# Optimization experiments

Measured on AMD Instinct MI355X. Metric: run time of the kernel, lower is better.

The kernel has to match this reference:

```python
import jax, jax.numpy as jnp
import numpy as np
from functools import partial

N_NODES = 100000
N_EDGES = 3200000
F_IN, H1, H2, C_OUT = 128, 64, 32, 2


def setup_inputs() -> dict:
    key = jax.random.key(0)
    ks = jax.random.split(key, 8)
    x = jax.random.normal(ks[0], (N_NODES, F_IN), dtype=jnp.float32)
    edge_index = jax.random.randint(ks[1], (2, N_EDGES), 0, N_NODES, dtype=jnp.int64)
    def glorot(k, fan_in, fan_out):
        s = jnp.sqrt(6.0 / (fan_in + fan_out))
        return jax.random.uniform(k, (fan_in, fan_out), jnp.float32, -s, s)
    return {
        "x": x,
        "edge_index": edge_index,
        "W1": glorot(ks[2], F_IN, H1), "b1": jnp.zeros((H1,), jnp.float32),
        "W2": glorot(ks[3], H1, H2),   "b2": jnp.zeros((H2,), jnp.float32),
        "W3": glorot(ks[4], H2, C_OUT), "b3": jnp.zeros((C_OUT,), jnp.float32),
    }


def _gcn_norm(edge_index, num_nodes):
    # add self-loops, compute symmetric normalization D^{-1/2} (A+I) D^{-1/2}
    loop = jnp.arange(num_nodes, dtype=edge_index.dtype)
    src = jnp.concatenate([edge_index[0], loop])
    dst = jnp.concatenate([edge_index[1], loop])
    deg = jax.ops.segment_sum(jnp.ones_like(dst, dtype=jnp.float32), dst,
                              num_segments=num_nodes)
    dinv = jax.lax.rsqrt(deg)  # deg >= 1 because of self-loops
    norm = dinv[src] * dinv[dst]  # [E + N]
    return src, dst, norm


def _gcn_conv(x, W, b, src, dst, norm, num_nodes):
    # PyG GCNConv: linear transform, then normalized scatter-aggregate, then bias
    xw = x @ W                                   # [N, F_out]
    msg = xw[src] * norm[:, None]                # [E+N, F_out] gather + scale
    out = jax.ops.segment_sum(msg, dst, num_segments=num_nodes)
    return out + b


def reference(x, edge_index, W1, b1, W2, b2, W3, b3):
    n = x.shape[0]
    src, dst, norm = _gcn_norm(edge_index, n)
    h = jax.nn.relu(_gcn_conv(x, W1, b1, src, dst, norm, n))
    # dropout is identity in eval mode
    h = jax.nn.relu(_gcn_conv(h, W2, b2, src, dst, norm, n))
    h = _gcn_conv(h, W3, b3, src, dst, norm, n)
    return jax.nn.log_softmax(h, axis=1)
```

## Files before the change

### kernel.cpp

```cpp
#include <hip/hip_runtime.h>
#include <hip/hip_bf16.h>
#include <math.h>

constexpr int N = 100000;
constexpr int E = 3200000;
constexpr int FIN = 128, H1 = 64, H2 = 32, COUT = 2;

constexpr int BUK_SHIFT = 8;
constexpr int BUK_NODES = 256;
constexpr int NBUK = (N + BUK_NODES - 1) / BUK_NODES;
constexpr int CAP = 10240;
constexpr int MS_TPB = 1024;
constexpr int MS_EPT = 12;
constexpr int CHUNK = MS_TPB * MS_EPT;
constexpr int MS_WGS = (E + CHUNK - 1) / CHUNK;

__global__ void k_initcur(int* __restrict__ gcursor) {
    int i = blockIdx.x * blockDim.x + threadIdx.x;
    if (i < NBUK) gcursor[i] = i * CAP;
}

__global__ __launch_bounds__(MS_TPB)
void k_mslice(const int* __restrict__ src, const int* __restrict__ dst,
              int* __restrict__ gcursor, unsigned* __restrict__ ebuf) {
    __shared__ int cnt[NBUK];
    __shared__ int base[NBUK];
    const int t = threadIdx.x;
    for (int i = t; i < NBUK; i += MS_TPB) cnt[i] = 0;
    __syncthreads();
    const int e0 = blockIdx.x * CHUNK;

    int rb[MS_EPT];
    unsigned rv[MS_EPT];
#pragma unroll
    for (int j = 0; j < MS_EPT; ++j) {
        int e = e0 + j * MS_TPB + t;
        if (e < E) {
            int d = dst[e];
            int b = d >> BUK_SHIFT;
            rb[j] = b;
            rv[j] = (unsigned)src[e] | ((unsigned)(d & (BUK_NODES - 1)) << 17);
            atomicAdd(&cnt[b], 1);
        } else {
            rb[j] = -1; rv[j] = 0;
        }
    }
    __syncthreads();
    for (int i = t; i < NBUK; i += MS_TPB) {
        int c = cnt[i];
        base[i] = c ? atomicAdd(&gcursor[i], c) : 0;
    }
    __syncthreads();
    for (int i = t; i < NBUK; i += MS_TPB) cnt[i] = 0;
    __syncthreads();
#pragma unroll
    for (int j = 0; j < MS_EPT; ++j) {
        int b = rb[j];
        if (b >= 0) {
            int r = atomicAdd(&cnt[b], 1);
            int p = base[b] + r;
            if (p < (b + 1) * CAP) ebuf[p] = rv[j];
        }
    }
}

__global__ __launch_bounds__(512)
void k_bscan(const int* __restrict__ gcursor, int* __restrict__ bbase,
             int* __restrict__ rowptr) {
    __shared__ int sm[512];
    const int t = threadIdx.x;
    int v = (t < NBUK) ? (gcursor[t] - t * CAP) : 0;
    sm[t] = v;
    __syncthreads();
    for (int off = 1; off < 512; off <<= 1) {
        int cur = sm[t];
        int add = (t >= off) ? sm[t - off] : 0;
        __syncthreads();
        sm[t] = cur + add;
        __syncthreads();
    }
    if (t < NBUK) bbase[t] = sm[t] - v;
    if (t == 0) { bbase[NBUK] = E; rowptr[N] = E; }
}

__global__ __launch_bounds__(256)
void k_build(const int* __restrict__ gcursor, const int* __restrict__ bbase,
             const unsigned* __restrict__ ebuf, int* __restrict__ rowptr,
             float* __restrict__ dinv, int* __restrict__ csr_src) {
    __shared__ unsigned ent[CAP];
    __shared__ int cnt[BUK_NODES];
    __shared__ int sm[BUK_NODES];
    __shared__ int cur[BUK_NODES];
    const int b = blockIdx.x;
    const int t = threadIdx.x;
    const int fill = gcursor[b] - b * CAP;
    const int gsrc = b * CAP;
    const int gdst = bbase[b];

    cnt[t] = 0;
    __syncthreads();
    for (int j = t; j < fill; j += 256) {
        unsigned v = ebuf[gsrc + j];
        ent[j] = v;
        atomicAdd(&cnt[v >> 17], 1);
    }
    __syncthreads();
    sm[t] = cnt[t];
    __syncthreads();
    for (int off = 1; off < BUK_NODES; off <<= 1) {
        int cv = sm[t];
        int add = (t >= off) ? sm[t - off] : 0;
        __syncthreads();
        sm[t] = cv + add;
        __syncthreads();
    }
    {
        int ex = sm[t] - cnt[t];
        cur[t] = gdst + ex;
        int node = (b << BUK_SHIFT) + t;
        if (node < N) {
            rowptr[node] = gdst + ex;
            dinv[node] = rsqrtf((float)cnt[t] + 1.0f);
        }
    }
    __syncthreads();
    for (int j = t; j < fill; j += 256) {
        unsigned v = ent[j];
        int p = atomicAdd(&cur[v >> 17], 1);
        csr_src[p] = (int)(v & 0x1FFFFu);
    }
}

template<int FI, int FO>
__global__ __launch_bounds__(256)
void k_gemm_tile_bf(const float* __restrict__ h, const float* __restrict__ Wg,
                    const float* __restrict__ dinv, __hip_bfloat16* __restrict__ y) {
    constexpr int TX  = FO / 4;
    constexpr int TY  = 256 / TX;
    constexpr int RPT = 64 / TY;
    constexpr int XS  = 68;
    constexpr int KQ  = FI / 4;

    __shared__ float xsT[FI][XS];

    const int tid = threadIdx.x;
    const int tx = tid % TX;
    const int ty = tid / TX;
    const int row0 = blockIdx.x * 64;

    for (int idx = tid; idx < 64 * KQ; idx += 256) {
        int g   = idx / 8;
        int rlo = idx % 8;
        int k4  = g % KQ;
        int rhi = g / KQ;
        int r   = rlo + 8 * rhi;
        int row = row0 + r;
        float4 v = make_float4(0.f, 0.f, 0.f, 0.f);
        if (row < N) v = *(const float4*)(h + (size_t)row * FI + 4 * k4);
        xsT[4 * k4 + 0][r] = v.x;
        xsT[4 * k4 + 1][r] = v.y;
        xsT[4 * k4 + 2][r] = v.z;
        xsT[4 * k4 + 3][r] = v.w;
    }
    __syncthreads();

    float acc[RPT][4];
#pragma unroll
    for (int i = 0; i < RPT; ++i)
#pragma unroll
        for (int c = 0; c < 4; ++c) acc[i][c] = 0.0f;

#pragma unroll 4
    for (int k = 0; k < FI; ++k) {
        const float4 wv = *(const float4*)(Wg + (size_t)k * FO + 4 * tx);
        float xv[RPT];
        if constexpr (RPT == 4) {
            float4 t = *(const float4*)&xsT[k][4 * ty];
            xv[0] = t.x; xv[1] = t.y; xv[2] = t.z; xv[3] = t.w;
        } else {
            float2 t = *(const float2*)&xsT[k][2 * ty];
            xv[0] = t.x; xv[1] = t.y;
        }
#pragma unroll
        for (int i = 0; i < RPT; ++i) {
            acc[i][0] = fmaf(xv[i], wv.x, acc[i][0]);
            acc[i][1] = fmaf(xv[i], wv.y, acc[i][1]);
            acc[i][2] = fmaf(xv[i], wv.z, acc[i][2]);
            acc[i][3] = fmaf(xv[i], wv.w, acc[i][3]);
        }
    }

#pragma unroll
    for (int i = 0; i < RPT; ++i) {
        int row = row0 + ty * RPT + i;
        if (row >= N) continue;
        float di = dinv[row];
        auto cvt = [](float f) -> unsigned short {
            __hip_bfloat16 b = __float2bfloat16(f);
            return *reinterpret_cast<unsigned short*>(&b);
        };
        ushort4 pk;
        pk.x = cvt(di * acc[i][0]);
        pk.y = cvt(di * acc[i][1]);
        pk.z = cvt(di * acc[i][2]);
        pk.w = cvt(di * acc[i][3]);
        *(ushort4*)&y[(size_t)row * FO + 4 * tx] = pk;
    }
}

template<int FI, int FO, int ROWS>
__global__ __launch_bounds__(FO * ROWS)
void k_gemm_scale(const float* __restrict__ h, const float* __restrict__ W,
                  const float* __restrict__ dinv, float* __restrict__ y) {
    __shared__ float xs[ROWS][FI];
    const int j = threadIdx.x;
    const int r = threadIdx.y;
    const int row0 = blockIdx.x * ROWS;
    const int tid = r * FO + j;
    constexpr int NT = FO * ROWS;
    for (int t = tid; t < ROWS * FI; t += NT) {
        int rr = t / FI, kk = t % FI;
        int row = row0 + rr;
        xs[rr][kk] = (row < N) ? h[(size_t)row * FI + kk] : 0.0f;
    }
    __syncthreads();
    const int row = row0 + r;
    if (row >= N) return;
    float acc = 0.0f;
#pragma unroll
    for (int k = 0; k < FI; ++k)
        acc = fmaf(xs[r][k], W[k * FO + j], acc);
    y[(size_t)row * FO + j] = dinv[row] * acc;
}

template<int F, bool RELU>
__global__ __launch_bounds__(256)
void k_aggregate_bf(const int* __restrict__ rowptr, const int* __restrict__ csr_src,
                    const __hip_bfloat16* __restrict__ y, const float* __restrict__ dinv,
                    const float* __restrict__ b, float* __restrict__ out) {
    constexpr int LPN = F / 2;
    constexpr int NPB = 256 / LPN;
    const int fp = threadIdx.x;
    const int n = blockIdx.x * NPB + threadIdx.y;
    if (n >= N) return;
    const unsigned* yw = (const unsigned*)y;

    auto load2 = [&](int s) -> float2 {
        unsigned u = yw[(size_t)s * LPN + fp];
        float2 v;
        v.x = __uint_as_float(u << 16);
        v.y = __uint_as_float(u & 0xffff0000u);
        return v;
    };

    float2 acc = load2(n);
    const int j0 = rowptr[n], j1 = rowptr[n + 1];
    int j = j0;
    for (; j + 8 <= j1; j += 8) {
        int s0 = csr_src[j],     s1 = csr_src[j + 1], s2 = csr_src[j + 2], s3 = csr_src[j + 3];
        int s4 = csr_src[j + 4], s5 = csr_src[j + 5], s6 = csr_src[j + 6], s7 = csr_src[j + 7];
        float2 v0 = load2(s0), v1 = load2(s1), v2 = load2(s2), v3 = load2(s3);
        float2 v4 = load2(s4), v5 = load2(s5), v6 = load2(s6), v7 = load2(s7);
        acc.x += ((v0.x + v1.x) + (v2.x + v3.x)) + ((v4.x + v5.x) + (v6.x + v7.x));
        acc.y += ((v0.y + v1.y) + (v2.y + v3.y)) + ((v4.y + v5.y) + (v6.y + v7.y));
    }
    for (; j < j1; ++j) {
        float2 v = load2(csr_src[j]);
        acc.x += v.x; acc.y += v.y;
    }
    const float di = dinv[n];
    float o0 = fmaf(di, acc.x, b[2 * fp]);
    float o1 = fmaf(di, acc.y, b[2 * fp + 1]);
    if (RELU) { o0 = fmaxf(o0, 0.0f); o1 = fmaxf(o1, 0.0f); }
    float2 res; res.x = o0; res.y = o1;
    *(float2*)&out[(size_t)n * F + 2 * fp] = res;
}

__global__ __launch_bounds__(256)
void k_final(const int* __restrict__ rowptr, const int* __restrict__ csr_src,
             const float* __restrict__ y, const float* __restrict__ dinv,
             const float* __restrict__ b, float* __restrict__ out) {
    const int c = threadIdx.x;
    const int n = blockIdx.x * 128 + threadIdx.y;
    float z = 0.0f;
    if (n < N) {
        const int j0 = rowptr[n], j1 = rowptr[n + 1];
        float acc = y[2 * n + c];
        int j = j0;
        for (; j + 4 <= j1; j += 4) {
            int s0 = csr_src[j], s1 = csr_src[j + 1], s2 = csr_src[j + 2], s3 = csr_src[j + 3];
            float a0 = y[2 * s0 + c], a1 = y[2 * s1 + c];
            float a2 = y[2 * s2 + c], a3 = y[2 * s3 + c];
            acc += (a0 + a1) + (a2 + a3);
        }
        for (; j < j1; ++j) acc += y[2 * csr_src[j] + c];
        z = fmaf(dinv[n], acc, b[c]);
    }
    float zo = __shfl_xor(z, 1);
    if (n < N) {
        float m = fmaxf(z, zo);
        float lse = m + logf(expf(z - m) + expf(zo - m));
        out[2 * n + c] = z - lse;
    }
}

extern "C" void kernel_launch(void* const* d_in, const int* in_sizes, int n_in,
                              void* d_out, int out_size, void* d_ws, size_t ws_size,
                              hipStream_t stream) {
    const float* x   = (const float*)d_in[0];
    const int*   ei  = (const int*)d_in[1];
    const float* W1  = (const float*)d_in[2];
    const float* b1  = (const float*)d_in[3];
    const float* W2  = (const float*)d_in[4];
    const float* b2  = (const float*)d_in[5];
    const float* W3  = (const float*)d_in[6];
    const float* b3  = (const float*)d_in[7];
    float* out = (float*)d_out;

    const int* src = ei;
    const int* dst = ei + E;

    char* p = (char*)d_ws;
    int*   rowptr  = (int*)p;   p += (size_t)(N + 1) * 4;
    float* dinv    = (float*)p; p += (size_t)N * 4;
    int*   gcursor = (int*)p;   p += (size_t)NBUK * 4;
    int*   bbase   = (int*)p;   p += (size_t)(NBUK + 1) * 4;
    int*   csr_src = (int*)p;   p += (size_t)E * 4;
    char*  bufA    = p;         p += (size_t)N * 64 * 4;
    char*  bufB    = p;         p += (size_t)N * 64 * 4;

    unsigned*       ebuf  = (unsigned*)bufA;
    __hip_bfloat16* y1    = (__hip_bfloat16*)bufA;
    float*          h1    = (float*)bufB;
    __hip_bfloat16* y2    = (__hip_bfloat16*)bufA;
    float*          h2    = (float*)(bufA + (size_t)N * H2 * 2);
    float*          y3    = (float*)bufB;

    k_initcur<<<(NBUK + 255) / 256, 256, 0, stream>>>(gcursor);
    k_mslice <<<MS_WGS, MS_TPB, 0, stream>>>(src, dst, gcursor, ebuf);
    k_bscan  <<<1, 512, 0, stream>>>(gcursor, bbase, rowptr);
    k_build  <<<NBUK, 256, 0, stream>>>(gcursor, bbase, ebuf, rowptr, dinv, csr_src);

    k_gemm_tile_bf<FIN, H1><<<(N + 63) / 64, 256, 0, stream>>>(x, W1, dinv, y1);
    k_aggregate_bf<H1, true><<<(N + 7) / 8, dim3(32, 8), 0, stream>>>(rowptr, csr_src, y1, dinv, b1, h1);

    k_gemm_tile_bf<H1, H2><<<(N + 63) / 64, 256, 0, stream>>>(h1, W2, dinv, y2);
    k_aggregate_bf<H2, true><<<(N + 15) / 16, dim3(16, 16), 0, stream>>>(rowptr, csr_src, y2, dinv, b2, h2);

    k_gemm_scale<H2, COUT, 128><<<(N + 127) / 128, dim3(COUT, 128), 0, stream>>>(h2, W3, dinv, y3);
    k_final<<<(N + 127) / 128, dim3(2, 128), 0, stream>>>(rowptr, csr_src, y3, dinv, b3, out);
}
```

Baseline: 386.7 us.

## Segment CSR by source range per bucket and aggregate per bucket block

After: 449.5 us. 16.2% more time.

```diff
diff --git a/kernel.cpp b/kernel.cpp
--- a/kernel.cpp
+++ b/kernel.cpp
@@ -6,12 +6,17 @@
 constexpr int E = 3200000;
 constexpr int FIN = 128, H1 = 64, H2 = 32, COUT = 2;
 
-constexpr int BUK_SHIFT = 8;
-constexpr int BUK_NODES = 256;
+constexpr int BUK_SHIFT = 6;
+constexpr int BUK_NODES = 64;
 constexpr int NBUK = (N + BUK_NODES - 1) / BUK_NODES;
-constexpr int CAP = 10240;
+constexpr int CAP = 2560;
+constexpr int SEG_SHIFT = 14;
+constexpr int NSEG = 7;
+constexpr int KEYS = NSEG * BUK_NODES;
+constexpr int RSTR = KEYS + 1;
+
 constexpr int MS_TPB = 1024;
-constexpr int MS_EPT = 12;
+constexpr int MS_EPT = 24;
 constexpr int CHUNK = MS_TPB * MS_EPT;
 constexpr int MS_WGS = (E + CHUNK - 1) / CHUNK;
 
@@ -64,70 +69,60 @@
     }
 }
 
-__global__ __launch_bounds__(512)
-void k_bscan(const int* __restrict__ gcursor, int* __restrict__ bbase,
-             int* __restrict__ rowptr) {
-    __shared__ int sm[512];
-    const int t = threadIdx.x;
-    int v = (t < NBUK) ? (gcursor[t] - t * CAP) : 0;
-    sm[t] = v;
-    __syncthreads();
-    for (int off = 1; off < 512; off <<= 1) {
-        int cur = sm[t];
-        int add = (t >= off) ? sm[t - off] : 0;
-        __syncthreads();
-        sm[t] = cur + add;
-        __syncthreads();
-    }
-    if (t < NBUK) bbase[t] = sm[t] - v;
-    if (t == 0) { bbase[NBUK] = E; rowptr[N] = E; }
-}
-
 __global__ __launch_bounds__(256)
-void k_build(const int* __restrict__ gcursor, const int* __restrict__ bbase,
-             const unsigned* __restrict__ ebuf, int* __restrict__ rowptr,
-             float* __restrict__ dinv, int* __restrict__ csr_src) {
+void k_build(const int* __restrict__ gcursor, unsigned* __restrict__ ebuf,
+             int* __restrict__ rptr, float* __restrict__ dinv) {
     __shared__ unsigned ent[CAP];
-    __shared__ int cnt[BUK_NODES];
-    __shared__ int sm[BUK_NODES];
-    __shared__ int cur[BUK_NODES];
+    __shared__ int cnt[512];
+    __shared__ int sa[512];
+    __shared__ int sb[512];
+    __shared__ int cur[512];
     const int b = blockIdx.x;
     const int t = threadIdx.x;
     const int fill = gcursor[b] - b * CAP;
-    const int gsrc = b * CAP;
-    const int gdst = bbase[b];
-
-    cnt[t] = 0;
+    const int gbase = b * CAP;
+
+    cnt[t] = 0; cnt[t + 256] = 0;
     __syncthreads();
     for (int j = t; j < fill; j += 256) {
-        unsigned v = ebuf[gsrc + j];
+        unsigned v = ebuf[gbase + j];
         ent[j] = v;
-        atomicAdd(&cnt[v >> 17], 1);
-    }
-    __syncthreads();
-    sm[t] = cnt[t];
-    __syncthreads();
-    for (int off = 1; off < BUK_NODES; off <<= 1) {
-        int cv = sm[t];
-        int add = (t >= off) ? sm[t - off] : 0;
+        int key = (int)((v & 0x1FFFFu) >> SEG_SHIFT) * BUK_NODES + (int)(v >> 17);
+        atomicAdd(&cnt[key], 1);
+    }
+    __syncthreads();
+    sa[t] = cnt[t]; sa[t + 256] = cnt[t + 256];
+    __syncthreads();
+    int* pin = sa; int* pout = sb;
+    for (int off = 1; off < 512; off <<= 1) {
+        pout[t]       = pin[t]       + ((t >= off)       ? pin[t - off]       : 0);
+        pout[t + 256] = pin[t + 256] + ((t + 256 >= off) ? pin[t + 256 - off] : 0);
         __syncthreads();
-        sm[t] = cv + add;
-        __syncthreads();
+        int* tmp = pin; pin = pout; pout = tmp;
     }
     {
-        int ex = sm[t] - cnt[t];
-        cur[t] = gdst + ex;
+        int ex0 = pin[t] - cnt[t];
+        int ex1 = pin[t + 256] - cnt[t + 256];
+        cur[t] = gbase + ex0;
+        cur[t + 256] = gbase + ex1;
+        if (t < KEYS) rptr[b * RSTR + t] = gbase + ex0;
+        int k2 = t + 256;
+        if (k2 < KEYS) rptr[b * RSTR + k2] = gbase + ex1;
+        if (t == 0) rptr[b * RSTR + KEYS] = gbase + fill;
+    }
+    if (t < BUK_NODES) {
+        int deg = 0;
+#pragma unroll
+        for (int s = 0; s < NSEG; ++s) deg += cnt[s * BUK_NODES + t];
         int node = (b << BUK_SHIFT) + t;
-        if (node < N) {
-            rowptr[node] = gdst + ex;
-            dinv[node] = rsqrtf((float)cnt[t] + 1.0f);
-        }
+        if (node < N) dinv[node] = rsqrtf((float)deg + 1.0f);
     }
     __syncthreads();
     for (int j = t; j < fill; j += 256) {
         unsigned v = ent[j];
-        int p = atomicAdd(&cur[v >> 17], 1);
-        csr_src[p] = (int)(v & 0x1FFFFu);
+        int key = (int)((v & 0x1FFFFu) >> SEG_SHIFT) * BUK_NODES + (int)(v >> 17);
+        int p = atomicAdd(&cur[key], 1);
+        ebuf[p] = v & 0x1FFFFu;
     }
 }
 
@@ -235,14 +230,17 @@
 
 template<int F, bool RELU>
 __global__ __launch_bounds__(256)
-void k_aggregate_bf(const int* __restrict__ rowptr, const int* __restrict__ csr_src,
-                    const __hip_bfloat16* __restrict__ y, const float* __restrict__ dinv,
-                    const float* __restrict__ b, float* __restrict__ out) {
-    constexpr int LPN = F / 2;
-    constexpr int NPB = 256 / LPN;
+void k_agg_seg(const int* __restrict__ rptr, const unsigned* __restrict__ csr,
+               const __hip_bfloat16* __restrict__ y, const float* __restrict__ dinv,
+               const float* __restrict__ bias, float* __restrict__ out) {
+    constexpr int LPN  = F / 2;
+    constexpr int NPY  = 256 / LPN;
+    constexpr int NPT  = BUK_NODES / NPY;
     const int fp = threadIdx.x;
-    const int n = blockIdx.x * NPB + threadIdx.y;
-    if (n >= N) return;
+    const int ty = threadIdx.y;
+    const int b = blockIdx.x;
+    const int base = b << BUK_SHIFT;
+    const int rbase = b * RSTR;
     const unsigned* yw = (const unsigned*)y;
 
     auto load2 = [&](int s) -> float2 {
@@ -253,48 +251,71 @@
         return v;
     };
 
-    float2 acc = load2(n);
-    const int j0 = rowptr[n], j1 = rowptr[n + 1];
-    int j = j0;
-    for (; j + 8 <= j1; j += 8) {
-        int s0 = csr_src[j],     s1 = csr_src[j + 1], s2 = csr_src[j + 2], s3 = csr_src[j + 3];
-        int s4 = csr_src[j + 4], s5 = csr_src[j + 5], s6 = csr_src[j + 6], s7 = csr_src[j + 7];
-        float2 v0 = load2(s0), v1 = load2(s1), v2 = load2(s2), v3 = load2(s3);
-        float2 v4 = load2(s4), v5 = load2(s5), v6 = load2(s6), v7 = load2(s7);
-        acc.x += ((v0.x + v1.x) + (v2.x + v3.x)) + ((v4.x + v5.x) + (v6.x + v7.x));
-        acc.y += ((v0.y + v1.y) + (v2.y + v3.y)) + ((v4.y + v5.y) + (v6.y + v7.y));
-    }
-    for (; j < j1; ++j) {
-        float2 v = load2(csr_src[j]);
-        acc.x += v.x; acc.y += v.y;
-    }
-    const float di = dinv[n];
-    float o0 = fmaf(di, acc.x, b[2 * fp]);
-    float o1 = fmaf(di, acc.y, b[2 * fp + 1]);
-    if (RELU) { o0 = fmaxf(o0, 0.0f); o1 = fmaxf(o1, 0.0f); }
-    float2 res; res.x = o0; res.y = o1;
-    *(float2*)&out[(size_t)n * F + 2 * fp] = res;
+    float2 acc[NPT];
+#pragma unroll
+    for (int i = 0; i < NPT; ++i) { acc[i].x = 0.0f; acc[i].y = 0.0f; }
+
+    for (int seg = 0; seg < NSEG; ++seg) {
+#pragma unroll
+        for (int i = 0; i < NPT; ++i) {
+            const int ld = ty + NPY * i;
+            const int k = seg * BUK_NODES + ld;
+            int j  = rptr[rbase + k];
+            const int j1 = rptr[rbase + k + 1];
+            float2 a = acc[i];
+            for (; j + 4 <= j1; j += 4) {
+                int s0 = (int)csr[j], s1 = (int)csr[j + 1];
+                int s2 = (int)csr[j + 2], s3 = (int)csr[j + 3];
+                float2 v0 = load2(s0), v1 = load2(s1), v2 = load2(s2), v3 = load2(s3);
+                a.x += (v0.x + v1.x) + (v2.x + v3.x);
+                a.y += (v0.y + v1.y) + (v2.y + v3.y);
+            }
+            for (; j < j1; ++j) {
+                float2 v = load2((int)csr[j]);
+                a.x += v.x; a.y += v.y;
+            }
+            acc[i] = a;
+        }
+    }
+
+    const float b0 = bias[2 * fp], b1 = bias[2 * fp + 1];
+#pragma unroll
+    for (int i = 0; i < NPT; ++i) {
+        const int node = base + ty + NPY * i;
+        if (node >= N) continue;
+        float2 self = load2(node);
+        const float di = dinv[node];
+        float o0 = fmaf(di, acc[i].x + self.x, b0);
+        float o1 = fmaf(di, acc[i].y + self.y, b1);
+        if (RELU) { o0 = fmaxf(o0, 0.0f); o1 = fmaxf(o1, 0.0f); }
+        float2 res; res.x = o0; res.y = o1;
+        *(float2*)&out[(size_t)node * F + 2 * fp] = res;
+    }
 }
 
 __global__ __launch_bounds__(256)
-void k_final(const int* __restrict__ rowptr, const int* __restrict__ csr_src,
+void k_final(const int* __restrict__ rptr, const unsigned* __restrict__ csr,
              const float* __restrict__ y, const float* __restrict__ dinv,
-             const float* __restrict__ b, float* __restrict__ out) {
+             const float* __restrict__ bias, float* __restrict__ out) {
     const int c = threadIdx.x;
     const int n = blockIdx.x * 128 + threadIdx.y;
     float z = 0.0f;
     if (n < N) {
-        const int j0 = rowptr[n], j1 = rowptr[n + 1];
+        const int b = n >> BUK_SHIFT;
+        const int ld = n & (BUK_NODES - 1);
+        const int rbase = b * RSTR;
         float acc = y[2 * n + c];
-        int j = j0;
-        for (; j + 4 <= j1; j += 4) {
-            int s0 = csr_src[j], s1 = csr_src[j + 1], s2 = csr_src[j + 2], s3 = csr_src[j + 3];
-            float a0 = y[2 * s0 + c], a1 = y[2 * s1 + c];
-            float a2 = y[2 * s2 + c], a3 = y[2 * s3 + c];
-            acc += (a0 + a1) + (a2 + a3);
-        }
-        for (; j < j1; ++j) acc += y[2 * csr_src[j] + c];
-        z = fmaf(dinv[n], acc, b[c]);
+        for (int seg = 0; seg < NSEG; ++seg) {
+            const int k = seg * BUK_NODES + ld;
+            int j = rptr[rbase + k];
+            const int j1 = rptr[rbase + k + 1];
+            for (; j + 2 <= j1; j += 2) {
+                int s0 = (int)csr[j], s1 = (int)csr[j + 1];
+                acc += y[2 * s0 + c] + y[2 * s1 + c];
+            }
+            for (; j < j1; ++j) acc += y[2 * (int)csr[j] + c];
+        }
+        z = fmaf(dinv[n], acc, bias[c]);
     }
     float zo = __shfl_xor(z, 1);
     if (n < N) {
@@ -321,32 +342,29 @@
     const int* dst = ei + E;
 
     char* p = (char*)d_ws;
-    int*   rowptr  = (int*)p;   p += (size_t)(N + 1) * 4;
-    float* dinv    = (float*)p; p += (size_t)N * 4;
-    int*   gcursor = (int*)p;   p += (size_t)NBUK * 4;
-    int*   bbase   = (int*)p;   p += (size_t)(NBUK + 1) * 4;
-    int*   csr_src = (int*)p;   p += (size_t)E * 4;
-    char*  bufA    = p;         p += (size_t)N * 64 * 4;
-    char*  bufB    = p;         p += (size_t)N * 64 * 4;
-
-    unsigned*       ebuf  = (unsigned*)bufA;
-    __hip_bfloat16* y1    = (__hip_bfloat16*)bufA;
-    float*          h1    = (float*)bufB;
-    __hip_bfloat16* y2    = (__hip_bfloat16*)bufA;
-    float*          h2    = (float*)(bufA + (size_t)N * H2 * 2);
-    float*          y3    = (float*)bufB;
+    float*    dinv    = (float*)p;    p += (size_t)N * 4;
+    int*      gcursor = (int*)p;      p += (size_t)NBUK * 4;
+    int*      rptr    = (int*)p;      p += (size_t)NBUK * RSTR * 4;
+    unsigned* ebuf    = (unsigned*)p; p += (size_t)NBUK * CAP * 4;
+    char*     bufA    = p;            p += (size_t)N * 64 * 4;
+    char*     bufB    = p;            p += (size_t)N * 64 * 4;
+
+    __hip_bfloat16* y1 = (__hip_bfloat16*)bufA;
+    float*          h1 = (float*)bufB;
+    __hip_bfloat16* y2 = (__hip_bfloat16*)bufA;
+    float*          h2 = (float*)(bufA + (size_t)N * H2 * 2);
+    float*          y3 = (float*)bufB;
 
     k_initcur<<<(NBUK + 255) / 256, 256, 0, stream>>>(gcursor);
     k_mslice <<<MS_WGS, MS_TPB, 0, stream>>>(src, dst, gcursor, ebuf);
-    k_bscan  <<<1, 512, 0, stream>>>(gcursor, bbase, rowptr);
-    k_build  <<<NBUK, 256, 0, stream>>>(gcursor, bbase, ebuf, rowptr, dinv, csr_src);
+    k_build  <<<NBUK, 256, 0, stream>>>(gcursor, ebuf, rptr, dinv);
 
     k_gemm_tile_bf<FIN, H1><<<(N + 63) / 64, 256, 0, stream>>>(x, W1, dinv, y1);
-    k_aggregate_bf<H1, true><<<(N + 7) / 8, dim3(32, 8), 0, stream>>>(rowptr, csr_src, y1, dinv, b1, h1);
+    k_agg_seg<H1, true><<<NBUK, dim3(32, 8), 0, stream>>>(rptr, ebuf, y1, dinv, b1, h1);
 
     k_gemm_tile_bf<H1, H2><<<(N + 63) / 64, 256, 0, stream>>>(h1, W2, dinv, y2);
-    k_aggregate_bf<H2, true><<<(N + 15) / 16, dim3(16, 16), 0, stream>>>(rowptr, csr_src, y2, dinv, b2, h2);
+    k_agg_seg<H2, true><<<NBUK, dim3(16, 16), 0, stream>>>(rptr, ebuf, y2, dinv, b2, h2);
 
     k_gemm_scale<H2, COUT, 128><<<(N + 127) / 128, dim3(COUT, 128), 0, stream>>>(h2, W3, dinv, y3);
-    k_final<<<(N + 127) / 128, dim3(2, 128), 0, stream>>>(rowptr, csr_src, y3, dinv, b3, out);
-}
+    k_final<<<(N + 127) / 128, dim3(2, 128), 0, stream>>>(rptr, ebuf, y3, dinv, b3, out);
+}
```
